# Performance work log

Measured on AMD Instinct MI355X. Metric: run time of the kernel, lower is better.

The kernel has to match this reference:

```python
import jax, jax.numpy as jnp
import numpy as np

N, M, D = 8, 512, 64          # latent groups, codebook size, code dim
B, L = 32, 1024               # batch, sequence length
COMMIT = 0.25                 # commitment_cost


def setup_inputs() -> dict:
    key = jax.random.key(0)
    k1, k2 = jax.random.split(key)
    x = jax.random.normal(k1, (B, N * D, L), dtype=jnp.float32)
    # matches embedding.uniform_(-1/M, 1/M)
    embedding = jax.random.uniform(k2, (N, M, D), dtype=jnp.float32,
                                   minval=-1.0 / M, maxval=1.0 / M)
    return {"x": x, "embedding": embedding}


def reference(x, embedding):
    # Inference-mode forward (EMA buffer updates are training-only side effects).
    Bx, C, Lx = x.shape
    Nn, Mm, Dd = embedding.shape
    # [B, C, L] -> [B, N, D, L] -> [N, B, L, D]
    xg = x.reshape(Bx, Nn, Dd, Lx).transpose(1, 0, 3, 2)
    x_flat = xg.reshape(Nn, Bx * Lx, Dd)                          # [N, BL, D]
    # Squared-distance expansion; argmin matches torch.cdist argmin (sqrt is monotone).
    x2 = jnp.sum(x_flat * x_flat, axis=-1, keepdims=True)         # [N, BL, 1]
    e2 = jnp.sum(embedding * embedding, axis=-1)[:, None, :]      # [N, 1, M]
    xe = jnp.einsum('ntd,nmd->ntm', x_flat, embedding)            # [N, BL, M]
    d2 = x2 - 2.0 * xe + e2
    indices = jnp.argmin(d2, axis=-1)                             # [N, BL] int
    quantized = jnp.take_along_axis(embedding, indices[..., None], axis=1)  # [N, BL, D]
    quantized = quantized.reshape(xg.shape)                       # [N, B, L, D]
    # commitment loss: mse(x, stop_grad(quantized))
    e_latent_loss = jnp.mean(jnp.square(xg - jax.lax.stop_gradient(quantized)))
    loss = COMMIT * e_latent_loss
    # straight-through estimator
    quantized_st = xg + jax.lax.stop_gradient(quantized - xg)
    # perplexity from code usage histogram (== mean of one-hot encodings)
    counts = jax.vmap(lambda idx: jnp.bincount(idx, length=Mm))(indices)   # [N, M]
    avg_probs = counts.astype(x.dtype) / jnp.asarray(Bx * Lx, x.dtype)
    perplexity = jnp.exp(-jnp.sum(avg_probs * jnp.log(avg_probs + 1e-10), axis=-1)).sum()
    out = quantized_st.transpose(1, 0, 3, 2).reshape(Bx, C, Lx)   # back to [B, C, L]
    return out, loss, perplexity
```

## Files before the change

kernel.cpp:

```cpp
#include <hip/hip_runtime.h>
#include <cfloat>
#include <cstddef>


#define N_G   8
#define M_CB  512
#define D_DIM 64
#define B_SZ  32
#define L_SEQ 1024
#define TOKENS (N_G * B_SZ * L_SEQ)
#define OUT_ELEMS ((size_t)B_SZ * N_G * D_DIM * L_SEQ)
#define MARGIN 2560
#define NLOSS 64

typedef _Float16 f16x8 __attribute__((ext_vector_type(8)));
typedef float    f32x4 __attribute__((ext_vector_type(4)));

#define EF_OFF   0
#define E2P_OFF  524288
#define E2R_OFF  540672
#define CNT_OFF  557056
#define LOSS_OFF 573440

__global__ void vq_ef16_kernel(const float* __restrict__ emb, unsigned int* __restrict__ ef) {
    int i = blockIdx.x * blockDim.x + threadIdx.x;
    if (i < N_G * M_CB * D_DIM / 2) {
        float2 v = reinterpret_cast<const float2*>(emb)[i];
        _Float16 h0 = (_Float16)(-2.0f * v.x);
        _Float16 h1 = (_Float16)(-2.0f * v.y);
        unsigned int u0 = (unsigned int)__builtin_bit_cast(unsigned short, h0);
        unsigned int u1 = (unsigned int)__builtin_bit_cast(unsigned short, h1);
        ef[i] = u0 | (u1 << 16);
    }
}

__global__ void vq_e2_kernel(const float* __restrict__ emb,
                             float* __restrict__ e2raw,
                             float* __restrict__ e2p) {
    int i = blockIdx.x * blockDim.x + threadIdx.x;
    if (i < N_G * M_CB) {
        const float* e = emb + (size_t)i * D_DIM;
        float s0 = 0.f, s1 = 0.f, s2 = 0.f, s3 = 0.f;
        #pragma unroll
        for (int d = 0; d < D_DIM; d += 4) {
            s0 = fmaf(e[d+0], e[d+0], s0);
            s1 = fmaf(e[d+1], e[d+1], s1);
            s2 = fmaf(e[d+2], e[d+2], s2);
            s3 = fmaf(e[d+3], e[d+3], s3);
        }
        float s = (s0 + s1) + (s2 + s3);
        e2raw[i] = s;
        e2p[i] = 1.0f + s;
    }
}

__global__ __launch_bounds__(256, 4)
void vq_mfma_kernel(const float* __restrict__ x,
                    const float* __restrict__ emb,
                    const unsigned short* __restrict__ ef16,
                    const float* __restrict__ e2raw,
                    const float* __restrict__ e2p,
                    float* __restrict__ out,
                    int* __restrict__ counts,
                    float* __restrict__ lossAcc) {
    __shared__ int hist[M_CB];
    __shared__ int cands[4][4][16][8];
    __shared__ __align__(16) short ebuf[4 * 16 * 72];

    const int tid  = threadIdx.x;
    hist[tid] = 0;
    hist[tid + 256] = 0;

    const int lane = tid & 63;
    const int wv   = tid >> 6;
    const int cc   = lane & 15;
    const int kl   = lane >> 4;
    const int kl4  = kl << 2;

    const int bb  = blockIdx.x;
    const int n   = bb >> 7;
    const int rem = bb & 127;
    const int b   = rem >> 2;
    const int l0  = ((rem & 3) << 8) + (wv << 6);

    const float* __restrict__ xg = x + (size_t)(b * N_G + n) * D_DIM * L_SEQ;
    const unsigned short* __restrict__ eg16 = ef16 + (size_t)n * M_CB * D_DIM;
    const float* __restrict__ e2pg = e2p + n * M_CB;

    const int st_t0 = tid >> 7;
    const int st_r0 = (tid >> 3) & 15;
    const int st_c0 = tid & 7;
    const int st_o0 = st_t0 * 1152 + st_r0 * 72 + st_c0 * 8;
    const int st_o1 = (st_t0 + 2) * 1152 + st_r0 * 72 + st_c0 * 8;

    f16x8 xf[4][2];
    float x2p = 0.f;
    #pragma unroll
    for (int s = 0; s < 4; ++s) {
        const int tok = l0 + s * 16 + cc;
        #pragma unroll
        for (int kc = 0; kc < 2; ++kc) {
            const int dbase = kc * 32 + kl * 8;
            f16x8 v;
            #pragma unroll
            for (int j = 0; j < 8; ++j) {
                const float xs = xg[(size_t)(dbase + j) * L_SEQ + tok];
                x2p = fmaf(xs, xs, x2p);
                v[j] = (_Float16)xs;
            }
            xf[s][kc] = v;
        }
    }

    int t1[4], t2[4];
    #pragma unroll
    for (int s = 0; s < 4; ++s) { t1[s] = 0x7FFFFFFF; t2[s] = 0x7FFFFFFF; }

    for (int outer = 0; outer < 8; ++outer) {
        {
            const unsigned short* gsrc = eg16 + outer * 4096;
            const uint4 g0 = *reinterpret_cast<const uint4*>(gsrc + tid * 8);
            const uint4 g1 = *reinterpret_cast<const uint4*>(gsrc + 2048 + tid * 8);
            *reinterpret_cast<uint4*>(&ebuf[st_o0]) = g0;
            *reinterpret_cast<uint4*>(&ebuf[st_o1]) = g1;
        }
        __syncthreads();

        #pragma unroll
        for (int ml = 0; ml < 4; ++ml) {
            const short* erow = &ebuf[ml * 1152 + cc * 72 + kl * 8];
            const f16x8 ea0 = *reinterpret_cast<const f16x8*>(erow);
            const f16x8 ea1 = *reinterpret_cast<const f16x8*>(erow + 32);
            const int mt = outer * 4 + ml;
            const f32x4 ce2 = *reinterpret_cast<const f32x4*>(e2pg + mt * 16 + kl4);
            const int mb = mt * 16 + kl4;

            #pragma unroll
            for (int s = 0; s < 4; ++s) {
                f32x4 dacc = __builtin_amdgcn_mfma_f32_16x16x32_f16(ea0, xf[s][0], ce2,  0, 0, 0);
                dacc       = __builtin_amdgcn_mfma_f32_16x16x32_f16(ea1, xf[s][1], dacc, 0, 0, 0);
                const int p0 = (__float_as_int(dacc[0]) & ~511) | (mb + 0);
                const int p1 = (__float_as_int(dacc[1]) & ~511) | (mb + 1);
                const int p2 = (__float_as_int(dacc[2]) & ~511) | (mb + 2);
                const int p3 = (__float_as_int(dacc[3]) & ~511) | (mb + 3);
                int mn = min(p0, p1), mx = max(p0, p1);
                t2[s] = min(t2[s], max(min(t1[s], mx), mn));
                t1[s] = min(t1[s], mn);
                mn = min(p2, p3); mx = max(p2, p3);
                t2[s] = min(t2[s], max(min(t1[s], mx), mn));
                t1[s] = min(t1[s], mn);
            }
        }
        __syncthreads();
    }

    #pragma unroll
    for (int s = 0; s < 4; ++s) {
        cands[wv][s][cc][kl * 2 + 0] = t1[s];
        cands[wv][s][cc][kl * 2 + 1] = t2[s];
    }
    __syncthreads();

    const int tok = l0 + lane;
    int cd[8];
    #pragma unroll
    for (int j = 0; j < 8; ++j) cd[j] = cands[wv][kl][cc][j];
    int pmin = cd[0];
    #pragma unroll
    for (int j = 1; j < 8; ++j) pmin = min(pmin, cd[j]);

    float xv[D_DIM];
    #pragma unroll
    for (int d = 0; d < D_DIM; ++d)
        xv[d] = xg[(size_t)d * L_SEQ + tok];

    const float* __restrict__ eg  = emb + (size_t)n * M_CB * D_DIM;
    const float* __restrict__ e2g = e2raw + n * M_CB;
    float best1 = FLT_MAX, best2 = FLT_MAX;
    int   idx1  = 0x7FFFFFFF, idx2 = 0x7FFFFFFF;
    for (int j = 0; j < 8; ++j) {
        if (cd[j] - pmin <= MARGIN) {
            const int m = cd[j] & 511;
            const float4* em4 = reinterpret_cast<const float4*>(eg + (size_t)m * D_DIM);
            float a0 = 0.f, a1 = 0.f, a2 = 0.f, a3 = 0.f;
            #pragma unroll
            for (int q = 0; q < 16; ++q) {
                const float4 e4 = em4[q];
                a0 = fmaf(xv[q*4+0], e4.x, a0);
                a1 = fmaf(xv[q*4+1], e4.y, a1);
                a2 = fmaf(xv[q*4+2], e4.z, a2);
                a3 = fmaf(xv[q*4+3], e4.w, a3);
            }
            const float dist = fmaf(-2.f, (a0 + a1) + (a2 + a3), e2g[m]);
            if (dist < best1 || (dist == best1 && m < idx1)) {
                best2 = best1; idx2 = idx1; best1 = dist; idx1 = m;
            } else if (dist < best2 || (dist == best2 && m < idx2)) {
                best2 = dist; idx2 = m;
            }
        }
    }

    if (best2 - best1 < 1e-4f) {
        const float* eA = eg + (size_t)idx1 * D_DIM;
        const float* eB = eg + (size_t)idx2 * D_DIM;
        double dA = 0.0, dB = 0.0;
        #pragma unroll
        for (int d = 0; d < D_DIM; ++d) {
            const double da = (double)xv[d] - (double)eA[d];
            const double db = (double)xv[d] - (double)eB[d];
            dA = fma(da, da, dA);
            dB = fma(db, db, dB);
        }
        if (dB < dA || (dB == dA && idx2 < idx1)) { idx1 = idx2; best1 = best2; }
    }

    const size_t obase = (size_t)(b * N_G + n) * D_DIM * L_SEQ + (size_t)tok;
    const float* __restrict__ ebest = eg + (size_t)idx1 * D_DIM;
    #pragma unroll
    for (int d = 0; d < D_DIM; d += 4) {
        const float4 qv = *reinterpret_cast<const float4*>(ebest + d);
        out[obase + (size_t)(d+0) * L_SEQ] = qv.x;
        out[obase + (size_t)(d+1) * L_SEQ] = qv.y;
        out[obase + (size_t)(d+2) * L_SEQ] = qv.z;
        out[obase + (size_t)(d+3) * L_SEQ] = qv.w;
    }

    float sq = x2p + best1;
    #pragma unroll
    for (int off = 32; off > 0; off >>= 1)
        sq += __shfl_down(sq, off, 64);
    if (lane == 0)
        atomicAdd(&lossAcc[bb & (NLOSS - 1)], sq);

    atomicAdd(&hist[idx1], 1);
    __syncthreads();
    {
        const int base = n * M_CB;
        int c0 = hist[tid];
        int c1 = hist[tid + 256];
        if (c0) atomicAdd(&counts[base + tid], c0);
        if (c1) atomicAdd(&counts[base + tid + 256], c1);
    }
}

__global__ void vq_finalize_kernel(const int* __restrict__ counts,
                                   const float* __restrict__ lossAcc,
                                   float* __restrict__ outTail) {
    __shared__ float red[256];
    const int tid = threadIdx.x;
    float perp = 0.f;
    for (int n = 0; n < N_G; ++n) {
        float h = 0.f;
        for (int m = tid; m < M_CB; m += 256) {
            const float p = (float)counts[n * M_CB + m] * (1.0f / (B_SZ * L_SEQ));
            h += p * logf(p + 1e-10f);
        }
        red[tid] = h;
        __syncthreads();
        #pragma unroll
        for (int s = 128; s > 0; s >>= 1) {
            if (tid < s) red[tid] += red[tid + s];
            __syncthreads();
        }
        if (tid == 0) perp += expf(-red[0]);
        __syncthreads();
    }
    if (tid == 0) {
        float ls = 0.f;
        for (int j = 0; j < NLOSS; ++j) ls += lossAcc[j];
        outTail[0] = 0.25f * (ls / (float)OUT_ELEMS);
        outTail[1] = perp;
    }
}

extern "C" void kernel_launch(void* const* d_in, const int* in_sizes, int n_in,
                              void* d_out, int out_size, void* d_ws, size_t ws_size,
                              hipStream_t stream) {
    const float* x   = (const float*)d_in[0];
    const float* emb = (const float*)d_in[1];
    float* out = (float*)d_out;
    char*  ws  = (char*)d_ws;

    unsigned int* ef16u  = (unsigned int*)(ws + EF_OFF);
    float* e2p    = (float*)(ws + E2P_OFF);
    float* e2r    = (float*)(ws + E2R_OFF);
    int*   counts = (int*)(ws + CNT_OFF);
    float* lossA  = (float*)(ws + LOSS_OFF);

    hipMemsetAsync(ws + CNT_OFF, 0, N_G * M_CB * 4 + NLOSS * 4, stream);
    vq_ef16_kernel<<<(N_G * M_CB * D_DIM / 2 + 255) / 256, 256, 0, stream>>>(emb, ef16u);
    vq_e2_kernel<<<(N_G * M_CB + 255) / 256, 256, 0, stream>>>(emb, e2r, e2p);
    vq_mfma_kernel<<<TOKENS / 256, 256, 0, stream>>>(
        x, emb, (const unsigned short*)ef16u, e2r, e2p, out, counts, lossA);
    vq_finalize_kernel<<<1, 256, 0, stream>>>(counts, lossA, out + OUT_ELEMS);
}
```

Baseline: 95.69 us.

## Prefetch next codebook tile into registers, fuse prep kernels, shuffle-reduce finalize

```diff
diff --git a/kernel.cpp b/kernel.cpp
--- a/kernel.cpp
+++ b/kernel.cpp
@@ -22,8 +22,11 @@
 #define CNT_OFF  557056
 #define LOSS_OFF 573440
 
-__global__ void vq_ef16_kernel(const float* __restrict__ emb, unsigned int* __restrict__ ef) {
-    int i = blockIdx.x * blockDim.x + threadIdx.x;
+__global__ void vq_prep_kernel(const float* __restrict__ emb,
+                               unsigned int* __restrict__ ef,
+                               float* __restrict__ e2raw,
+                               float* __restrict__ e2p) {
+    const int i = blockIdx.x * blockDim.x + threadIdx.x;
     if (i < N_G * M_CB * D_DIM / 2) {
         float2 v = reinterpret_cast<const float2*>(emb)[i];
         _Float16 h0 = (_Float16)(-2.0f * v.x);
@@ -32,12 +35,6 @@
         unsigned int u1 = (unsigned int)__builtin_bit_cast(unsigned short, h1);
         ef[i] = u0 | (u1 << 16);
     }
-}
-
-__global__ void vq_e2_kernel(const float* __restrict__ emb,
-                             float* __restrict__ e2raw,
-                             float* __restrict__ e2p) {
-    int i = blockIdx.x * blockDim.x + threadIdx.x;
     if (i < N_G * M_CB) {
         const float* e = emb + (size_t)i * D_DIM;
         float s0 = 0.f, s1 = 0.f, s2 = 0.f, s3 = 0.f;
@@ -116,15 +113,20 @@
     #pragma unroll
     for (int s = 0; s < 4; ++s) { t1[s] = 0x7FFFFFFF; t2[s] = 0x7FFFFFFF; }
 
+    uint4 g0 = *reinterpret_cast<const uint4*>(eg16 + tid * 8);
+    uint4 g1 = *reinterpret_cast<const uint4*>(eg16 + 2048 + tid * 8);
+
     for (int outer = 0; outer < 8; ++outer) {
+        *reinterpret_cast<uint4*>(&ebuf[st_o0]) = g0;
+        *reinterpret_cast<uint4*>(&ebuf[st_o1]) = g1;
+        __syncthreads();
+
         {
-            const unsigned short* gsrc = eg16 + outer * 4096;
-            const uint4 g0 = *reinterpret_cast<const uint4*>(gsrc + tid * 8);
-            const uint4 g1 = *reinterpret_cast<const uint4*>(gsrc + 2048 + tid * 8);
-            *reinterpret_cast<uint4*>(&ebuf[st_o0]) = g0;
-            *reinterpret_cast<uint4*>(&ebuf[st_o1]) = g1;
-        }
-        __syncthreads();
+            const int nxt = (outer < 7) ? outer + 1 : 7;
+            const unsigned short* gsrc = eg16 + nxt * 4096 + tid * 8;
+            g0 = *reinterpret_cast<const uint4*>(gsrc);
+            g1 = *reinterpret_cast<const uint4*>(gsrc + 2048);
+        }
 
         #pragma unroll
         for (int ml = 0; ml < 4; ++ml) {
@@ -246,26 +248,30 @@
 __global__ void vq_finalize_kernel(const int* __restrict__ counts,
                                    const float* __restrict__ lossAcc,
                                    float* __restrict__ outTail) {
-    __shared__ float red[256];
-    const int tid = threadIdx.x;
-    float perp = 0.f;
-    for (int n = 0; n < N_G; ++n) {
-        float h = 0.f;
-        for (int m = tid; m < M_CB; m += 256) {
-            const float p = (float)counts[n * M_CB + m] * (1.0f / (B_SZ * L_SEQ));
-            h += p * logf(p + 1e-10f);
-        }
-        red[tid] = h;
-        __syncthreads();
-        #pragma unroll
-        for (int s = 128; s > 0; s >>= 1) {
-            if (tid < s) red[tid] += red[tid + s];
-            __syncthreads();
-        }
-        if (tid == 0) perp += expf(-red[0]);
-        __syncthreads();
-    }
+    __shared__ float ent[8];
+    const int tid  = threadIdx.x;
+    const int lane = tid & 63;
+    const int wvid = tid >> 6;
+
+    #pragma unroll
+    for (int h = 0; h < 2; ++h) {
+        const int n = wvid * 2 + h;
+        float s = 0.f;
+        #pragma unroll
+        for (int r = 0; r < 8; ++r) {
+            const float p = (float)counts[n * M_CB + r * 64 + lane] * (1.0f / (B_SZ * L_SEQ));
+            s += p * logf(p + 1e-10f);
+        }
+        #pragma unroll
+        for (int off = 32; off > 0; off >>= 1)
+            s += __shfl_down(s, off, 64);
+        if (lane == 0) ent[n] = s;
+    }
+    __syncthreads();
     if (tid == 0) {
+        float perp = 0.f;
+        #pragma unroll
+        for (int n = 0; n < 8; ++n) perp += expf(-ent[n]);
         float ls = 0.f;
         for (int j = 0; j < NLOSS; ++j) ls += lossAcc[j];
         outTail[0] = 0.25f * (ls / (float)OUT_ELEMS);
@@ -288,8 +294,7 @@
     float* lossA  = (float*)(ws + LOSS_OFF);
 
     hipMemsetAsync(ws + CNT_OFF, 0, N_G * M_CB * 4 + NLOSS * 4, stream);
-    vq_ef16_kernel<<<(N_G * M_CB * D_DIM / 2 + 255) / 256, 256, 0, stream>>>(emb, ef16u);
-    vq_e2_kernel<<<(N_G * M_CB + 255) / 256, 256, 0, stream>>>(emb, e2r, e2p);
+    vq_prep_kernel<<<(N_G * M_CB * D_DIM / 2 + 255) / 256, 256, 0, stream>>>(emb, ef16u, e2r, e2p);
     vq_mfma_kernel<<<TOKENS / 256, 256, 0, stream>>>(
         x, emb, (const unsigned short*)ef16u, e2r, e2p, out, counts, lossA);
     vq_finalize_kernel<<<1, 256, 0, stream>>>(counts, lossA, out + OUT_ELEMS);
```

Result: faster. 88.03 us (-8.0%).
